# Kernel tuning notes

Measured on AMD Instinct MI355X. Metric: run time of the kernel, lower is better.

Reference implementation:

```python
import jax, jax.numpy as jnp
import numpy as np

NUM_HEADS = 8
KEY_DIM = 16
D = 32          # attn_ratio * key_dim
DH = D * NUM_HEADS  # 256
NH_KD = KEY_DIM * NUM_HEADS  # 128
DIM = 256


def _conv1x1_bn(x, W, s, b):
    # 1x1 conv (no bias) followed by eval-mode BatchNorm folded to affine.
    # x: [B, Cin, H, W], W: [Cout, Cin], s/b: [Cout]
    y = jnp.einsum('oc,bchw->bohw', W, x)
    return y * s[None, :, None, None] + b[None, :, None, None]


def setup_inputs() -> dict:
    key = jax.random.key(0)
    ks = jax.random.split(key, 16)
    B, C, H, Wd = 2, DIM, 64, 64
    rgb = jax.random.normal(ks[0], (B, C, H, Wd), dtype=jnp.float32)
    edge = jax.random.normal(ks[1], (B, C, H, Wd), dtype=jnp.float32)

    def conv_w(k, o, i):
        return jax.random.normal(k, (o, i), dtype=jnp.float32) * (1.0 / np.sqrt(i))

    def bn(k, c):
        k1, k2 = jax.random.split(k)
        s = jax.random.uniform(k1, (c,), dtype=jnp.float32, minval=0.5, maxval=1.5)
        b = jax.random.normal(k2, (c,), dtype=jnp.float32) * 0.1
        return s, b

    Wq = conv_w(ks[2], NH_KD, C); sq, bq = bn(ks[3], NH_KD)
    Wk = conv_w(ks[4], NH_KD, C); sk, bk = bn(ks[5], NH_KD)
    Wv = conv_w(ks[6], DH, C);   sv, bv = bn(ks[7], DH)
    Wp = conv_w(ks[8], C, DH);   sp, bp = bn(ks[9], C)
    return dict(rgb=rgb, edge=edge, Wq=Wq, sq=sq, bq=bq, Wk=Wk, sk=sk, bk=bk,
                Wv=Wv, sv=sv, bv=bv, Wp=Wp, sp=sp, bp=bp)


def reference(rgb, edge, Wq, sq, bq, Wk, sk, bk, Wv, sv, bv, Wp, sp, bp):
    B, C, H, Wd = rgb.shape
    N = H * Wd
    # Q from rgb, K/V from edge (all 1x1 conv + BN)
    qq = _conv1x1_bn(rgb, Wq, sq, bq).reshape(B, NUM_HEADS, KEY_DIM, N)
    qq = jnp.transpose(qq, (0, 1, 3, 2))                       # [B,h,N,kd]
    kk = _conv1x1_bn(edge, Wk, sk, bk).reshape(B, NUM_HEADS, KEY_DIM, N)  # [B,h,kd,N]
    vv = _conv1x1_bn(edge, Wv, sv, bv).reshape(B, NUM_HEADS, D, N)
    vv = jnp.transpose(vv, (0, 1, 3, 2))                       # [B,h,N,d]
    # NOTE: original forward does NOT apply self.scale -- faithful omission.
    attn = jnp.einsum('bhnk,bhkm->bhnm', qq, kk)               # [B,h,N,N]
    attn = jax.nn.softmax(attn, axis=-1)
    xx = jnp.einsum('bhnm,bhmd->bhnd', attn, vv)               # [B,h,N,d]
    xx = jnp.transpose(xx, (0, 1, 3, 2)).reshape(B, DH, H, Wd)
    xx = jax.nn.relu(xx)                                       # activation before proj conv
    xx = _conv1x1_bn(xx, Wp, sp, bp)                           # [B,C,H,W]
    return xx
```

## Files before the change

kernel.cpp:

```cpp
#include <hip/hip_runtime.h>
#include <hip/hip_bf16.h>

#define NB 2
#define CIN 256
#define NPIX 4096
#define NHEADS 8
#define KD 16
#define DV 32
#define DH 256
#define NHKD 128

typedef short bf16x8 __attribute__((ext_vector_type(8)));
typedef short s16x4 __attribute__((ext_vector_type(4)));
typedef float f32x2 __attribute__((ext_vector_type(2)));
typedef float f32x4 __attribute__((ext_vector_type(4)));
typedef float f32x16 __attribute__((ext_vector_type(16)));
typedef unsigned int u32x2 __attribute__((ext_vector_type(2)));
typedef unsigned int u32x4 __attribute__((ext_vector_type(4)));

#define LOG2E 1.4426950408889634f

static __device__ __forceinline__ unsigned short f2bf(float f) {
    __hip_bfloat16 h = __float2bfloat16(f);
    return __builtin_bit_cast(unsigned short, h);
}

static __device__ __forceinline__ unsigned pack_rhu(float lo, float hi) {
    unsigned a = __builtin_bit_cast(unsigned, lo) + 0x8000u;
    unsigned b = __builtin_bit_cast(unsigned, hi) + 0x8000u;
    return (a >> 16) | (b & 0xffff0000u);
}

static __device__ __forceinline__ unsigned pack_rn(float lo, float hi) {
    float2 t; t.x = lo; t.y = hi;
    __hip_bfloat162 b2 = __float22bfloat162_rn(t);
    unsigned r;
    __builtin_memcpy(&r, &b2, 4);
    return r;
}

__global__ __launch_bounds__(256) void k_prep(
    const float* __restrict__ Wq, const float* __restrict__ Wk,
    const float* __restrict__ Wv, const float* __restrict__ Wp,
    unsigned short* __restrict__ wq, unsigned short* __restrict__ wk,
    unsigned short* __restrict__ wv, unsigned short* __restrict__ wp)
{
    int i = blockIdx.x * 256 + threadIdx.x;
    if (i < NHKD * CIN) { wq[i] = f2bf(Wq[i]); wk[i] = f2bf(Wk[i]); }
    if (i < DH * CIN)   { wv[i] = f2bf(Wv[i]); wp[i] = f2bf(Wp[i]); }
}

__global__ __launch_bounds__(256) void k_qkv(
    const float* __restrict__ rgb, const float* __restrict__ edge,
    const unsigned short* __restrict__ wq, const unsigned short* __restrict__ wk,
    const unsigned short* __restrict__ wv,
    const float* __restrict__ sq, const float* __restrict__ bq,
    const float* __restrict__ sk, const float* __restrict__ bk,
    const float* __restrict__ sv, const float* __restrict__ bv,
    unsigned short* __restrict__ Qw, unsigned short* __restrict__ Kw,
    unsigned short* __restrict__ Vw)
{
    const int nb = blockIdx.x;
    const int ob = blockIdx.y;
    const int b  = blockIdx.z;
    const int tid = threadIdx.x;
    const int wave = tid >> 6, lane = tid & 63;
    const int cl = lane & 15, g = lane >> 4;

    const float* X; const unsigned short* W; const float* sc; const float* bi;
    int obase, job;
    if (ob < 2)      { X = rgb  + (size_t)b*CIN*NPIX; W = wq; sc = sq; bi = bq; obase = ob*64;     job = 0; }
    else if (ob < 4) { X = edge + (size_t)b*CIN*NPIX; W = wk; sc = sk; bi = bk; obase = (ob-2)*64; job = 1; }
    else             { X = edge + (size_t)b*CIN*NPIX; W = wv; sc = sv; bi = bv; obase = (ob-4)*64; job = 2; }

    __shared__ float xt[32 * 65];

    f32x4 acc[4];
    #pragma unroll
    for (int i = 0; i < 4; i++) acc[i] = (f32x4)0.f;

    const int n0 = nb * 64;
    const int ow = obase + wave * 16 + cl;
    const unsigned short* Wrow = W + (size_t)ow * CIN;

    for (int kt = 0; kt < 8; kt++) {
        __syncthreads();
        {
            int tr = tid >> 6;
            int tc = tid & 63;
            #pragma unroll
            for (int r = 0; r < 8; r++) {
                int c_local = r * 4 + tr;
                xt[c_local * 65 + tc] = X[(size_t)(kt * 32 + c_local) * NPIX + n0 + tc];
            }
        }
        __syncthreads();
        #pragma unroll
        for (int ns = 0; ns < 4; ns++) {
            u32x4 aw;
            #pragma unroll
            for (int w = 0; w < 4; w++)
                aw[w] = pack_rhu(xt[(8 * g + 2 * w) * 65 + ns * 16 + cl],
                                 xt[(8 * g + 2 * w + 1) * 65 + ns * 16 + cl]);
            bf16x8 a = __builtin_bit_cast(bf16x8, aw);
            bf16x8 wfrag = *reinterpret_cast<const bf16x8*>(Wrow + kt * 32 + 8 * g);
            acc[ns] = __builtin_amdgcn_mfma_f32_16x16x32_bf16(a, wfrag, acc[ns], 0, 0, 0);
        }
    }

    const float sco = sc[ow], bio = bi[ow];
    if (job == 2) {
        int h = ow >> 5, d = ow & 31;
        unsigned short* dst = Vw + ((size_t)((b * 8 + h) * 32 + d)) * NPIX;
        #pragma unroll
        for (int ns = 0; ns < 4; ns++) {
            int nr = n0 + ns * 16 + 4 * g;
            s16x4 pk;
            #pragma unroll
            for (int r = 0; r < 4; r++) pk[r] = (short)f2bf(acc[ns][r] * sco + bio);
            *reinterpret_cast<s16x4*>(dst + nr) = pk;
        }
    } else {
        float scq = sco, biq = bio;
        if (job == 0) { scq *= LOG2E; biq *= LOG2E; }
        const int gp = (job == 1) ? (((g & 1) << 1) | (g >> 1)) : g;
        unsigned short* base = (job == 0) ? Qw : Kw;
        int h = ow >> 4, kd = ow & 15;
        unsigned short* dst = base + ((size_t)(b * 8 + h) * NPIX) * KD + kd;
        #pragma unroll
        for (int ns = 0; ns < 4; ns++)
            #pragma unroll
            for (int r = 0; r < 4; r++) {
                int nr = n0 + ns * 16 + 4 * gp + r;
                dst[(size_t)nr * KD] = f2bf(acc[ns][r] * scq + biq);
            }
    }
}

typedef const unsigned int __attribute__((address_space(1)))* gp_t;
typedef unsigned int __attribute__((address_space(3)))* lp_t;

__global__ __launch_bounds__(256, 6) void k_attn(
    const unsigned short* __restrict__ Qw, const unsigned short* __restrict__ Kw,
    const unsigned short* __restrict__ Vw, unsigned short* __restrict__ Ow)
{
    const int id = blockIdx.x;
    const int bh = (id & 7) * 2 + ((id >> 3) & 1);
    const int qg = id >> 4;
    const int tid = threadIdx.x;
    const int wave = tid >> 6, lane = tid & 63;
    const int l31 = lane & 31, hi = lane >> 5;

    __shared__ union {
        unsigned short v[4][2080];
        struct { float o[4][32][32]; float l[4][32]; } c;
    } sh;

    const unsigned short* Kbase = Kw + (size_t)bh * NPIX * KD;
    const unsigned short* Vbase = Vw + (size_t)bh * DV * NPIX;

    const int q0 = qg * 32;
    const bf16x8 qf = *(const bf16x8*)(Qw + ((size_t)bh * NPIX + q0 + l31) * KD + 8 * hi);

    const unsigned short* Kln = Kbase + (size_t)l31 * KD + 8 * hi;
#define KF0(T) (*(const bf16x8*)(Kln + ((T) * 64 + 0) * KD))
#define KF1(T) (*(const bf16x8*)(Kln + ((T) * 64 + 32) * KD))

    const int scb = ((lane & 7) * 16) ^ ((lane >> 3) << 4);
    const unsigned short* Vln = Vbase + (size_t)(lane >> 3) * NPIX + (scb >> 1);
#define STAGE(T) do { _Pragma("unroll") for (int j = 0; j < 4; ++j) \
    __builtin_amdgcn_global_load_lds( \
        (gp_t)(const void*)(Vln + (size_t)j * 8 * NPIX + (size_t)(T) * 64), \
        (lp_t)(void*)(&sh.v[wave][j * 520]), 16, 0, 0); } while (0)

    const int vsw = (l31 & 7) << 4;
    const int vbase = (l31 >> 3) * 520 + (l31 & 7) * 64;

    f32x16 o = (f32x16)0.f;
    float l_run = 0.f;
    const f32x16 z16 = (f32x16)0.f;

    const int T0 = wave * 16;

    #pragma unroll
    for (int t = 0; t < 16; ++t) {
        const int T = T0 + t;
        bf16x8 ka0 = KF0(T);
        bf16x8 ka1 = KF1(T);
        asm volatile("s_waitcnt lgkmcnt(0)" ::: "memory");
        STAGE(T);

        __builtin_amdgcn_s_setprio(1);
        f32x16 s0 = __builtin_amdgcn_mfma_f32_32x32x16_bf16(ka0, qf, z16, 0, 0, 0);
        __builtin_amdgcn_s_setprio(0);
        #pragma unroll
        for (int i = 0; i < 16; ++i) s0[i] = __builtin_amdgcn_exp2f(s0[i]);
        {
            f32x2 p[4];
            #pragma unroll
            for (int j = 0; j < 4; ++j) {
                f32x2 a = {s0[2*j], s0[2*j+1]};
                f32x2 b = {s0[2*j+8], s0[2*j+9]};
                p[j] = a + b;
            }
            p[0] += p[2]; p[1] += p[3]; p[0] += p[1];
            l_run += p[0].x + p[0].y;
        }
        unsigned u0[8];
        #pragma unroll
        for (int ss = 0; ss < 8; ++ss) u0[ss] = pack_rn(s0[2*ss], s0[2*ss+1]);

        asm volatile("s_waitcnt vmcnt(0)" ::: "memory");

        __builtin_amdgcn_s_setprio(1);
        {
            u32x4 av;
            av.x = u0[0]; av.y = u0[1]; av.z = u0[2]; av.w = u0[3];
            const int vi0 = vbase + (((16 * hi) ^ vsw) >> 1);
            bf16x8 vb0 = *(const bf16x8*)(&sh.v[wave][vi0]);
            o = __builtin_amdgcn_mfma_f32_32x32x16_bf16(__builtin_bit_cast(bf16x8, av), vb0, o, 0, 0, 0);
            av.x = u0[4]; av.y = u0[5]; av.z = u0[6]; av.w = u0[7];
            const int vi1 = vbase + (((32 + 16 * hi) ^ vsw) >> 1);
            bf16x8 vb1 = *(const bf16x8*)(&sh.v[wave][vi1]);
            o = __builtin_amdgcn_mfma_f32_32x32x16_bf16(__builtin_bit_cast(bf16x8, av), vb1, o, 0, 0, 0);
        }
        __builtin_amdgcn_s_setprio(0);

        __builtin_amdgcn_s_setprio(1);
        f32x16 s1 = __builtin_amdgcn_mfma_f32_32x32x16_bf16(ka1, qf, z16, 0, 0, 0);
        __builtin_amdgcn_s_setprio(0);
        #pragma unroll
        for (int i = 0; i < 16; ++i) s1[i] = __builtin_amdgcn_exp2f(s1[i]);
        {
            f32x2 p[4];
            #pragma unroll
            for (int j = 0; j < 4; ++j) {
                f32x2 a = {s1[2*j], s1[2*j+1]};
                f32x2 b = {s1[2*j+8], s1[2*j+9]};
                p[j] = a + b;
            }
            p[0] += p[2]; p[1] += p[3]; p[0] += p[1];
            l_run += p[0].x + p[0].y;
        }
        unsigned u1[8];
        #pragma unroll
        for (int ss = 0; ss < 8; ++ss) u1[ss] = pack_rn(s1[2*ss], s1[2*ss+1]);

        __builtin_amdgcn_s_setprio(1);
        {
            u32x4 av;
            av.x = u1[0]; av.y = u1[1]; av.z = u1[2]; av.w = u1[3];
            const int vi2 = vbase + (((64 + 16 * hi) ^ vsw) >> 1);
            bf16x8 vb2 = *(const bf16x8*)(&sh.v[wave][vi2]);
            o = __builtin_amdgcn_mfma_f32_32x32x16_bf16(__builtin_bit_cast(bf16x8, av), vb2, o, 0, 0, 0);
            av.x = u1[4]; av.y = u1[5]; av.z = u1[6]; av.w = u1[7];
            const int vi3 = vbase + (((96 + 16 * hi) ^ vsw) >> 1);
            bf16x8 vb3 = *(const bf16x8*)(&sh.v[wave][vi3]);
            o = __builtin_amdgcn_mfma_f32_32x32x16_bf16(__builtin_bit_cast(bf16x8, av), vb3, o, 0, 0, 0);
        }
        __builtin_amdgcn_s_setprio(0);
    }
#undef KF0
#undef KF1
#undef STAGE

    l_run += __shfl_xor(l_run, 32, 64);

    __syncthreads();
    #pragma unroll
    for (int r = 0; r < 16; ++r) {
        const int qr = (r & 3) + 8 * (r >> 2) + 4 * hi;
        sh.c.o[wave][qr][l31] = o[r];
    }
    if (hi == 0) sh.c.l[wave][l31] = l_run;
    __syncthreads();

    const int q = tid >> 3;
    const int d0 = (tid & 7) * 4;
    const float lsum = sh.c.l[0][q] + sh.c.l[1][q] + sh.c.l[2][q] + sh.c.l[3][q];
    const float linv = __builtin_amdgcn_rcpf(lsum);
    f32x4 s4 = *(const f32x4*)(&sh.c.o[0][q][d0]);
    s4 += *(const f32x4*)(&sh.c.o[1][q][d0]);
    s4 += *(const f32x4*)(&sh.c.o[2][q][d0]);
    s4 += *(const f32x4*)(&sh.c.o[3][q][d0]);
    float v[4];
    #pragma unroll
    for (int i = 0; i < 4; ++i) v[i] = fmaxf(s4[i] * linv, 0.f);
    const int b = bh >> 3, h = bh & 7;
    u32x2 pk;
    pk.x = (unsigned)f2bf(v[0]) | ((unsigned)f2bf(v[1]) << 16);
    pk.y = (unsigned)f2bf(v[2]) | ((unsigned)f2bf(v[3]) << 16);
    *reinterpret_cast<u32x2*>(Ow + ((size_t)b * NPIX + q0 + q) * DH + h * DV + d0) = pk;
}

__global__ __launch_bounds__(256) void k_proj(
    const unsigned short* __restrict__ Xo, const unsigned short* __restrict__ wp,
    const float* __restrict__ sp, const float* __restrict__ bp,
    float* __restrict__ out)
{
    const int nb = blockIdx.x;
    const int b  = blockIdx.y;
    const int tid = threadIdx.x;
    const int wave = tid >> 6, lane = tid & 63;
    const int cl = lane & 15, g = lane >> 4;

    const int cbase = wave * 64;
    f32x4 acc[4][2];
    #pragma unroll
    for (int i = 0; i < 4; i++)
        #pragma unroll
        for (int j = 0; j < 2; j++) acc[i][j] = (f32x4)0.f;

    const unsigned short* Xb = Xo + ((size_t)b * NPIX + nb * 32) * DH;

    #pragma unroll
    for (int kt = 0; kt < 8; kt++) {
        bf16x8 afr[4];
        #pragma unroll
        for (int cs = 0; cs < 4; cs++)
            afr[cs] = *reinterpret_cast<const bf16x8*>(wp + (size_t)(cbase + cs * 16 + cl) * DH + kt * 32 + 8 * g);
        #pragma unroll
        for (int ns = 0; ns < 2; ns++) {
            bf16x8 bfr = *reinterpret_cast<const bf16x8*>(Xb + (size_t)(ns * 16 + cl) * DH + kt * 32 + 8 * g);
            #pragma unroll
            for (int cs = 0; cs < 4; cs++)
                acc[cs][ns] = __builtin_amdgcn_mfma_f32_16x16x32_bf16(afr[cs], bfr, acc[cs][ns], 0, 0, 0);
        }
    }

    #pragma unroll
    for (int cs = 0; cs < 4; cs++)
        #pragma unroll
        for (int r = 0; r < 4; r++) {
            int c = cbase + cs * 16 + 4 * g + r;
            float scv = sp[c], biv = bp[c];
            float* dst = out + ((size_t)b * DH + c) * NPIX + nb * 32;
            #pragma unroll
            for (int ns = 0; ns < 2; ns++)
                dst[ns * 16 + cl] = acc[cs][ns][r] * scv + biv;
        }
}

extern "C" void kernel_launch(void* const* d_in, const int* in_sizes, int n_in,
                              void* d_out, int out_size, void* d_ws, size_t ws_size,
                              hipStream_t stream) {
    const float* rgb  = (const float*)d_in[0];
    const float* edge = (const float*)d_in[1];
    const float* Wq = (const float*)d_in[2];
    const float* sq = (const float*)d_in[3];
    const float* bq = (const float*)d_in[4];
    const float* Wk = (const float*)d_in[5];
    const float* sk = (const float*)d_in[6];
    const float* bk = (const float*)d_in[7];
    const float* Wv = (const float*)d_in[8];
    const float* sv = (const float*)d_in[9];
    const float* bv = (const float*)d_in[10];
    const float* Wp = (const float*)d_in[11];
    const float* sp = (const float*)d_in[12];
    const float* bp = (const float*)d_in[13];
    float* out = (float*)d_out;

    char* ws = (char*)d_ws;
    unsigned short* wq = (unsigned short*)(ws + 0);
    unsigned short* wk = (unsigned short*)(ws + (64 << 10));
    unsigned short* wv = (unsigned short*)(ws + (128 << 10));
    unsigned short* wp = (unsigned short*)(ws + (256 << 10));
    size_t o = 384 << 10;
    unsigned short* Qw = (unsigned short*)(ws + o); o += (size_t)16 * NPIX * KD * 2;
    unsigned short* Kw = (unsigned short*)(ws + o); o += (size_t)16 * NPIX * KD * 2;
    unsigned short* Vw = (unsigned short*)(ws + o); o += (size_t)16 * DV * NPIX * 2;
    unsigned short* Ow = (unsigned short*)(ws + o);

    k_prep<<<dim3(256), dim3(256), 0, stream>>>(Wq, Wk, Wv, Wp, wq, wk, wv, wp);
    k_qkv<<<dim3(64, 8, NB), dim3(256), 0, stream>>>(rgb, edge, wq, wk, wv,
                                                     sq, bq, sk, bk, sv, bv, Qw, Kw, Vw);
    k_attn<<<dim3(2048), dim3(256), 0, stream>>>(Qw, Kw, Vw, Ow);
    k_proj<<<dim3(128, NB), dim3(256), 0, stream>>>(Ow, wp, sp, bp, out);
}
```

Baseline: 86.10 us.

## Double-buffer V tiles in LDS and prefetch next K fragments

```diff
diff --git a/kernel.cpp b/kernel.cpp
--- a/kernel.cpp
+++ b/kernel.cpp
@@ -140,7 +140,7 @@
 typedef const unsigned int __attribute__((address_space(1)))* gp_t;
 typedef unsigned int __attribute__((address_space(3)))* lp_t;
 
-__global__ __launch_bounds__(256, 6) void k_attn(
+__global__ __launch_bounds__(256) void k_attn(
     const unsigned short* __restrict__ Qw, const unsigned short* __restrict__ Kw,
     const unsigned short* __restrict__ Vw, unsigned short* __restrict__ Ow)
 {
@@ -152,7 +152,7 @@
     const int l31 = lane & 31, hi = lane >> 5;
 
     __shared__ union {
-        unsigned short v[4][2080];
+        unsigned short v[4][2][2048];
         struct { float o[4][32][32]; float l[4][32]; } c;
     } sh;
 
@@ -168,27 +168,31 @@
 
     const int scb = ((lane & 7) * 16) ^ ((lane >> 3) << 4);
     const unsigned short* Vln = Vbase + (size_t)(lane >> 3) * NPIX + (scb >> 1);
-#define STAGE(T) do { _Pragma("unroll") for (int j = 0; j < 4; ++j) \
+#define STAGE(T, BUF) do { _Pragma("unroll") for (int j = 0; j < 4; ++j) \
     __builtin_amdgcn_global_load_lds( \
         (gp_t)(const void*)(Vln + (size_t)j * 8 * NPIX + (size_t)(T) * 64), \
-        (lp_t)(void*)(&sh.v[wave][j * 520]), 16, 0, 0); } while (0)
+        (lp_t)(void*)(&sh.v[wave][BUF][j * 512]), 16, 0, 0); } while (0)
 
     const int vsw = (l31 & 7) << 4;
-    const int vbase = (l31 >> 3) * 520 + (l31 & 7) * 64;
 
     f32x16 o = (f32x16)0.f;
     float l_run = 0.f;
     const f32x16 z16 = (f32x16)0.f;
 
     const int T0 = wave * 16;
+    STAGE(T0, 0);
+    bf16x8 ka0 = KF0(T0), ka1 = KF1(T0);
+    bf16x8 kb0, kb1;
 
     #pragma unroll
     for (int t = 0; t < 16; ++t) {
         const int T = T0 + t;
-        bf16x8 ka0 = KF0(T);
-        bf16x8 ka1 = KF1(T);
-        asm volatile("s_waitcnt lgkmcnt(0)" ::: "memory");
-        STAGE(T);
+        const int cur = t & 1;
+        if (t < 15) {
+            STAGE(T + 1, cur ^ 1);
+            kb0 = KF0(T + 1);
+            kb1 = KF1(T + 1);
+        }
 
         __builtin_amdgcn_s_setprio(1);
         f32x16 s0 = __builtin_amdgcn_mfma_f32_32x32x16_bf16(ka0, qf, z16, 0, 0, 0);
@@ -210,18 +214,16 @@
         #pragma unroll
         for (int ss = 0; ss < 8; ++ss) u0[ss] = pack_rn(s0[2*ss], s0[2*ss+1]);
 
-        asm volatile("s_waitcnt vmcnt(0)" ::: "memory");
-
         __builtin_amdgcn_s_setprio(1);
         {
             u32x4 av;
             av.x = u0[0]; av.y = u0[1]; av.z = u0[2]; av.w = u0[3];
-            const int vi0 = vbase + (((16 * hi) ^ vsw) >> 1);
-            bf16x8 vb0 = *(const bf16x8*)(&sh.v[wave][vi0]);
+            const int vi0 = (l31 * 128 + ((16 * hi) ^ vsw)) >> 1;
+            bf16x8 vb0 = *(const bf16x8*)(&sh.v[wave][cur][vi0]);
             o = __builtin_amdgcn_mfma_f32_32x32x16_bf16(__builtin_bit_cast(bf16x8, av), vb0, o, 0, 0, 0);
             av.x = u0[4]; av.y = u0[5]; av.z = u0[6]; av.w = u0[7];
-            const int vi1 = vbase + (((32 + 16 * hi) ^ vsw) >> 1);
-            bf16x8 vb1 = *(const bf16x8*)(&sh.v[wave][vi1]);
+            const int vi1 = (l31 * 128 + ((32 + 16 * hi) ^ vsw)) >> 1;
+            bf16x8 vb1 = *(const bf16x8*)(&sh.v[wave][cur][vi1]);
             o = __builtin_amdgcn_mfma_f32_32x32x16_bf16(__builtin_bit_cast(bf16x8, av), vb1, o, 0, 0, 0);
         }
         __builtin_amdgcn_s_setprio(0);
@@ -250,15 +252,16 @@
         {
             u32x4 av;
             av.x = u1[0]; av.y = u1[1]; av.z = u1[2]; av.w = u1[3];
-            const int vi2 = vbase + (((64 + 16 * hi) ^ vsw) >> 1);
-            bf16x8 vb2 = *(const bf16x8*)(&sh.v[wave][vi2]);
+            const int vi2 = (l31 * 128 + ((64 + 16 * hi) ^ vsw)) >> 1;
+            bf16x8 vb2 = *(const bf16x8*)(&sh.v[wave][cur][vi2]);
             o = __builtin_amdgcn_mfma_f32_32x32x16_bf16(__builtin_bit_cast(bf16x8, av), vb2, o, 0, 0, 0);
             av.x = u1[4]; av.y = u1[5]; av.z = u1[6]; av.w = u1[7];
-            const int vi3 = vbase + (((96 + 16 * hi) ^ vsw) >> 1);
-            bf16x8 vb3 = *(const bf16x8*)(&sh.v[wave][vi3]);
+            const int vi3 = (l31 * 128 + ((96 + 16 * hi) ^ vsw)) >> 1;
+            bf16x8 vb3 = *(const bf16x8*)(&sh.v[wave][cur][vi3]);
             o = __builtin_amdgcn_mfma_f32_32x32x16_bf16(__builtin_bit_cast(bf16x8, av), vb3, o, 0, 0, 0);
         }
         __builtin_amdgcn_s_setprio(0);
+        ka0 = kb0; ka1 = kb1;
     }
 #undef KF0
 #undef KF1
```

After: 90.58 us. 5.2% more time.
